# Kernel tuning notes

Hardware: AMD Instinct MI355X
Metric: run time of the kernel (lower is better)

The kernel has to match this reference:

```python
import jax, jax.numpy as jnp
import numpy as np

N_NODES = 100000
N_EDGES = 1600000
IN_DIM = 128
HID_DIM = 32
OUT_DIM = 64
N_REL = 8
N_CLASSES = 2


def setup_inputs() -> dict:
    key = jax.random.key(0)
    ks = jax.random.split(key, 12)
    x = jax.random.normal(ks[0], (N_NODES, IN_DIM), dtype=jnp.float32)
    edge_index = jax.random.randint(ks[1], (2, N_EDGES), 0, N_NODES, dtype=jnp.int64)
    edge_type = jax.random.randint(ks[2], (N_EDGES,), 0, N_REL, dtype=jnp.int64)
    # FastRGCNConv params: per-relation weight W [R, in, out], root weight, bias
    def glorot(k, shape):
        fan_in, fan_out = shape[-2], shape[-1]
        s = jnp.sqrt(6.0 / (fan_in + fan_out))
        return jax.random.uniform(k, shape, jnp.float32, -s, s)
    W1 = glorot(ks[3], (N_REL, IN_DIM, HID_DIM))
    root1 = glorot(ks[4], (IN_DIM, HID_DIM))
    b1 = jnp.zeros((HID_DIM,), jnp.float32)
    W2 = glorot(ks[5], (N_REL, HID_DIM, OUT_DIM))
    root2 = glorot(ks[6], (HID_DIM, OUT_DIM))
    b2 = jnp.zeros((OUT_DIM,), jnp.float32)
    lin_w = glorot(ks[7], (OUT_DIM, N_CLASSES))
    lin_b = jnp.zeros((N_CLASSES,), jnp.float32)
    return {"x": x, "edge_index": edge_index, "edge_type": edge_type,
            "W1": W1, "root1": root1, "b1": b1,
            "W2": W2, "root2": root2, "b2": b2,
            "lin_w": lin_w, "lin_b": lin_b}


def _fast_rgcn_conv(x, W, root, b, src, dst, etype, n_nodes):
    """FastRGCNConv: per-relation transform, gather by (src, relation),
    mean-aggregate by destination, plus root transform and bias."""
    # Transform all nodes by all relation weights: [N, R, H]
    xW = jnp.einsum('nf,rfh->nrh', x, W)
    # Per-edge message: relation-specific transformed source feature [E, H]
    msg = xW[src, etype]
    agg = jax.ops.segment_sum(msg, dst, num_segments=n_nodes)
    deg = jax.ops.segment_sum(jnp.ones((src.shape[0],), x.dtype), dst,
                              num_segments=n_nodes)
    agg = agg / jnp.maximum(deg, 1.0)[:, None]  # mean aggregation
    return agg + x @ root + b


def reference(x, edge_index, edge_type, W1, root1, b1, W2, root2, b2, lin_w, lin_b):
    src, dst = edge_index[0], edge_index[1]
    n = x.shape[0]
    h = jax.nn.relu(_fast_rgcn_conv(x, W1, root1, b1, src, dst, edge_type, n))
    h = _fast_rgcn_conv(h, W2, root2, b2, src, dst, edge_type, n)
    return h @ lin_w + lin_b
```

## Files before the change

### kernel.cpp

```cpp
#include <hip/hip_runtime.h>

#define NN      100000
#define IN_DIM  128
#define HID     32
#define ODIM    64
#define L1C     288
#define L2K     288
#define NWGS    196
#define NCB     784
#define CCAP    40
#define RECCAP  2304
#define G2ST    296
#define PST     40
#define HST     40

using bf16x8 = __attribute__((ext_vector_type(8))) short;
using f32x4  = __attribute__((ext_vector_type(4))) float;

__device__ __forceinline__ float bf2f(short s) {
    unsigned int u = ((unsigned int)(unsigned short)s) << 16;
    float f; __builtin_memcpy(&f, &u, 4); return f;
}
__device__ __forceinline__ short f2bf(float f) {
    unsigned int u; __builtin_memcpy(&u, &f, 4);
    u += 0x7fffu + ((u >> 16) & 1u);
    return (short)(u >> 16);
}
__device__ __forceinline__ float ldf(const void* p, int i, int f32) {
    return f32 ? ((const float*)p)[i] : bf2f(((const short*)p)[i]);
}
__device__ __forceinline__ int ldi(const int* p, long long i, int i64) {
    return i64 ? p[2 * i] : p[(int)i];
}

__global__ __launch_bounds__(1024) void detect(const short* __restrict__ x,
                                               const short* __restrict__ W1,
                                               const short* __restrict__ r1,
                                               const short* __restrict__ W2,
                                               const short* __restrict__ r2,
                                               const short* __restrict__ lw,
                                               const int* __restrict__ ei,
                                               const int* __restrict__ et,
                                               int* __restrict__ flags) {
    __shared__ int cnt[8];
    if (threadIdx.x < 8) cnt[threadIdx.x] = 0;
    __syncthreads();
    const short* ptrs[6] = {x, W1, r1, W2, r2, lw};
    const int    nsmp[6] = {1024, 1024, 1024, 1024, 1024, 64};
    int t = threadIdx.x;
#pragma unroll
    for (int j = 0; j < 6; ++j) {
        if (t < nsmp[j]) {
            unsigned int s = (unsigned short)ptrs[j][2 * t];
            unsigned int e = (s >> 7) & 0xFF;
            if (e >= 140u || (e >= 1u && e <= 100u)) atomicAdd(&cnt[j], 1);
        }
    }
    if (t < 128) {
        if (ei[2 * t + 1] != 0) atomicAdd(&cnt[6], 1);
        if (et[2 * t + 1] != 0) atomicAdd(&cnt[7], 1);
    }
    __syncthreads();
    if (t == 0) {
        const int ns[6] = {1024, 1024, 1024, 1024, 1024, 64};
        for (int j = 0; j < 6; ++j) flags[j] = (cnt[j] * 4 > ns[j]) ? 1 : 0;
        flags[6] = (cnt[6] == 0) ? 1 : 0;
        flags[7] = (cnt[7] == 0) ? 1 : 0;
    }
}

__global__ __launch_bounds__(256) void prep_all(const void* __restrict__ W1,
                                                const void* __restrict__ root1,
                                                const void* __restrict__ W2,
                                                const void* __restrict__ root2,
                                                const short* __restrict__ b1,
                                                const short* __restrict__ b2,
                                                const void* __restrict__ lin_w,
                                                const short* __restrict__ lin_b,
                                                short* __restrict__ w1t,
                                                short* __restrict__ w2ct,
                                                short* __restrict__ smallc,
                                                const int* __restrict__ flags) {
    int gi = blockIdx.x * 256 + threadIdx.x;
    if (gi < L1C * IN_DIM) {
        int c = gi >> 7, f = gi & 127;
        float v;
        if (c < 256) { int r = c >> 5, h = c & 31; v = ldf(W1, (r * IN_DIM + f) * HID + h, flags[1]); }
        else         { v = ldf(root1, f * HID + (c - 256), flags[2]); }
        w1t[c * IN_DIM + f] = f2bf(v);
        return;
    }
    int i2 = gi - L1C * IN_DIM;
    if (i2 < ODIM * L2K) {
        int c = i2 / L2K, k = i2 % L2K;
        float v;
        if (k < 256) { int r = k >> 5, kk = k & 31; v = ldf(W2, (r * HID + kk) * ODIM + c, flags[3]); }
        else         { v = ldf(root2, (k - 256) * ODIM + c, flags[4]); }
        w2ct[c * L2K + k] = f2bf(v);
        return;
    }
    int i3 = i2 - ODIM * L2K;
    if (i3 < 256) {
        if (i3 < 32)        smallc[i3] = b1[i3];
        else if (i3 < 96)   smallc[i3] = b2[i3 - 32];
        else if (i3 < 224)  smallc[i3] = f2bf(ldf(lin_w, i3 - 96, flags[5]));
        else if (i3 < 226)  smallc[i3] = lin_b[i3 - 224];
    }
}

__global__ __launch_bounds__(1024) void scatter_coarse(const int* __restrict__ ei,
                                                       const int* __restrict__ et,
                                                       int* __restrict__ cnt,
                                                       int* __restrict__ seg, int E,
                                                       const int* __restrict__ flags) {
    __shared__ int cur[NCB];
    if (threadIdx.x < NCB) cur[threadIdx.x] = 0;
    __syncthreads();
    int i64 = flags[6], t64 = flags[7];
    int epw = (E + NWGS - 1) / NWGS;
    int lo = blockIdx.x * epw;
    int hi = lo + epw; if (hi > E) hi = E;
    for (int i = lo + threadIdx.x; i < hi; i += 1024) {
        int s = ldi(ei, i, i64);
        int d = ldi(ei, (long long)E + i, i64);
        int r = ldi(et, i, t64);
        int cb = d >> 7;
        int pos = atomicAdd(&cur[cb], 1);
        if (pos < CCAP)
            seg[(cb * NWGS + (int)blockIdx.x) * CCAP + pos] = ((d & 127) << 20) | (s << 3) | r;
    }
    __syncthreads();
    if (threadIdx.x < NCB) {
        int c = cur[threadIdx.x];
        cnt[blockIdx.x * NCB + threadIdx.x] = c < CCAP ? c : CCAP;
    }
}

__global__ __launch_bounds__(64) void cb_sum(const int* __restrict__ cnt,
                                             int* __restrict__ cbTot) {
    int cb = blockIdx.x, lane = threadIdx.x;
    int t = 0;
    for (int g = lane; g < NWGS; g += 64) t += cnt[g * NCB + cb];
#pragma unroll
    for (int o = 32; o > 0; o >>= 1) t += __shfl_down(t, o, 64);
    if (lane == 0) cbTot[cb] = t;
}

__global__ __launch_bounds__(1024) void cb_scan2(const int* __restrict__ cbTot,
                                                 int* __restrict__ cbBase,
                                                 int* __restrict__ off) {
    __shared__ int s[1024];
    int t = threadIdx.x;
    int v = (t < NCB) ? cbTot[t] : 0;
    s[t] = v; __syncthreads();
    for (int o = 1; o < 1024; o <<= 1) {
        int u = (t >= o) ? s[t - o] : 0;
        __syncthreads();
        s[t] += u;
        __syncthreads();
    }
    if (t < NCB) cbBase[t] = s[t] - v;
    if (t == NCB - 1) off[NN] = s[t];
}

__global__ __launch_bounds__(256) void build_cb(const int* __restrict__ cnt,
                                                const int* __restrict__ seg,
                                                const int* __restrict__ cbBase,
                                                int* __restrict__ off,
                                                float* __restrict__ inv_deg,
                                                int* __restrict__ packed) {
    __shared__ int cntl[NWGS], soff[NWGS];
    __shared__ int recs[RECCAP];
    __shared__ int degl[128], basel[128], kcur[128];
    __shared__ int stmp[256];
    int cb = blockIdx.x, tid = threadIdx.x;
    if (tid < NWGS) cntl[tid] = cnt[tid * NCB + cb];
    if (tid < 128) degl[tid] = 0;
    __syncthreads();
    int v = (tid < NWGS) ? cntl[tid] : 0;
    stmp[tid] = v; __syncthreads();
    for (int o = 1; o < 256; o <<= 1) {
        int u = (tid >= o) ? stmp[tid - o] : 0;
        __syncthreads();
        stmp[tid] += u;
        __syncthreads();
    }
    if (tid < NWGS) soff[tid] = stmp[tid] - v;
    int tot = stmp[255]; if (tot > RECCAP) tot = RECCAP;
    __syncthreads();
    int wave = tid >> 6, lane = tid & 63;
    for (int g = wave; g < NWGS; g += 4) {
        int c = cntl[g], b = soff[g];
        const int* sp = seg + (cb * NWGS + g) * CCAP;
        for (int e = lane; e < c; e += 64)
            if (b + e < RECCAP) recs[b + e] = sp[e];
    }
    __syncthreads();
    for (int i = tid; i < tot; i += 256) atomicAdd(&degl[recs[i] >> 20], 1);
    __syncthreads();
    int dv = (tid < 128) ? degl[tid] : 0;
    stmp[tid] = dv; __syncthreads();
    for (int o = 1; o < 128; o <<= 1) {
        int u = (tid >= o) ? stmp[tid - o] : 0;
        __syncthreads();
        stmp[tid] += u;
        __syncthreads();
    }
    int gbase = cbBase[cb];
    if (tid < 128) {
        int excl = stmp[tid] - dv;
        basel[tid] = excl;
        kcur[tid] = 0;
        int node = cb * 128 + tid;
        if (node < NN) {
            off[node] = gbase + excl;
            inv_deg[node] = 1.0f / (float)(dv > 1 ? dv : 1);
        }
    }
    __syncthreads();
    for (int i = tid; i < tot; i += 256) {
        int rec = recs[i];
        int n = rec >> 20;
        int p = atomicAdd(&kcur[n], 1);
        packed[gbase + basel[n] + p] = ((n & 15) << 24) | (rec & 0xFFFFF);
    }
}

__global__ __launch_bounds__(256) void gemm1(const void* __restrict__ x,
                                             const short* __restrict__ w1t,
                                             short* __restrict__ xw,
                                             const int* __restrict__ flags) {
    int wave = threadIdx.x >> 6, lane = threadIdx.x & 63;
    int m = lane & 15, quad = lane >> 4;
    int row0 = (blockIdx.x * 4 + wave) * 64;
    if (row0 >= NN) return;

    bf16x8 a[4][4];
    int fp32 = flags[0];
#pragma unroll
    for (int t = 0; t < 4; ++t) {
        int row = row0 + t * 16 + m;
        int rc = row < NN ? row : NN - 1;
        if (fp32) {
            const float* xr = (const float*)x + rc * IN_DIM + quad * 8;
#pragma unroll
            for (int kt = 0; kt < 4; ++kt) {
                const f32x4* q = (const f32x4*)(xr + kt * 32);
                f32x4 u0 = q[0], u1 = q[1];
                bf16x8 tt;
                tt[0] = f2bf(u0[0]); tt[1] = f2bf(u0[1]); tt[2] = f2bf(u0[2]); tt[3] = f2bf(u0[3]);
                tt[4] = f2bf(u1[0]); tt[5] = f2bf(u1[1]); tt[6] = f2bf(u1[2]); tt[7] = f2bf(u1[3]);
                a[t][kt] = tt;
            }
        } else {
            const short* xr = (const short*)x + rc * IN_DIM + quad * 8;
#pragma unroll
            for (int kt = 0; kt < 4; ++kt) a[t][kt] = *(const bf16x8*)(xr + kt * 32);
        }
    }

    for (int ct = 0; ct < 18; ++ct) {
        const short* wp = w1t + (ct * 16 + m) * IN_DIM + quad * 8;
        bf16x8 b[4];
#pragma unroll
        for (int kt = 0; kt < 4; ++kt) b[kt] = *(const bf16x8*)(wp + kt * 32);
#pragma unroll
        for (int t = 0; t < 4; ++t) {
            f32x4 acc = {0.f, 0.f, 0.f, 0.f};
#pragma unroll
            for (int kt = 0; kt < 4; ++kt)
                acc = __builtin_amdgcn_mfma_f32_16x16x32_bf16(a[t][kt], b[kt], acc, 0, 0, 0);
#pragma unroll
            for (int i = 0; i < 4; ++i) {
                int r = row0 + t * 16 + quad * 4 + i;
                if (r < NN) xw[r * L1C + ct * 16 + m] = f2bf(acc[i]);
            }
        }
    }
}

__global__ __launch_bounds__(256) void agg1(const short* __restrict__ xw,
                                            const int* __restrict__ off,
                                            const int* __restrict__ packed,
                                            const float* __restrict__ inv_deg,
                                            const short* __restrict__ smallc,
                                            short* __restrict__ h) {
    int lane = threadIdx.x & 31;
    int node = blockIdx.x * 8 + (threadIdx.x >> 5);
    if (node >= NN) return;
    int s = off[node], e = off[node + 1];
    float acc = 0.f;
    int i = s;
    for (; i + 7 < e; i += 8) {
        int pk0 = packed[i],     pk1 = packed[i + 1], pk2 = packed[i + 2], pk3 = packed[i + 3];
        int pk4 = packed[i + 4], pk5 = packed[i + 5], pk6 = packed[i + 6], pk7 = packed[i + 7];
        float v0 = bf2f(xw[((pk0 >> 3) & 0x1FFFF) * L1C + (pk0 & 7) * 32 + lane]);
        float v1 = bf2f(xw[((pk1 >> 3) & 0x1FFFF) * L1C + (pk1 & 7) * 32 + lane]);
        float v2 = bf2f(xw[((pk2 >> 3) & 0x1FFFF) * L1C + (pk2 & 7) * 32 + lane]);
        float v3 = bf2f(xw[((pk3 >> 3) & 0x1FFFF) * L1C + (pk3 & 7) * 32 + lane]);
        float v4 = bf2f(xw[((pk4 >> 3) & 0x1FFFF) * L1C + (pk4 & 7) * 32 + lane]);
        float v5 = bf2f(xw[((pk5 >> 3) & 0x1FFFF) * L1C + (pk5 & 7) * 32 + lane]);
        float v6 = bf2f(xw[((pk6 >> 3) & 0x1FFFF) * L1C + (pk6 & 7) * 32 + lane]);
        float v7 = bf2f(xw[((pk7 >> 3) & 0x1FFFF) * L1C + (pk7 & 7) * 32 + lane]);
        acc += ((v0 + v1) + (v2 + v3)) + ((v4 + v5) + (v6 + v7));
    }
    for (; i + 3 < e; i += 4) {
        int pk0 = packed[i], pk1 = packed[i + 1], pk2 = packed[i + 2], pk3 = packed[i + 3];
        float v0 = bf2f(xw[((pk0 >> 3) & 0x1FFFF) * L1C + (pk0 & 7) * 32 + lane]);
        float v1 = bf2f(xw[((pk1 >> 3) & 0x1FFFF) * L1C + (pk1 & 7) * 32 + lane]);
        float v2 = bf2f(xw[((pk2 >> 3) & 0x1FFFF) * L1C + (pk2 & 7) * 32 + lane]);
        float v3 = bf2f(xw[((pk3 >> 3) & 0x1FFFF) * L1C + (pk3 & 7) * 32 + lane]);
        acc += (v0 + v1) + (v2 + v3);
    }
    for (; i < e; ++i) {
        int pk = packed[i];
        acc += bf2f(xw[((pk >> 3) & 0x1FFFF) * L1C + (pk & 7) * 32 + lane]);
    }
    float v = acc * inv_deg[node] + bf2f(xw[node * L1C + 256 + lane]) + bf2f(smallc[lane]);
    h[node * HID + lane] = f2bf(v > 0.f ? v : 0.f);
}

__global__ __launch_bounds__(256) void agg2_fused(const short* __restrict__ h,
                                                  const int* __restrict__ off,
                                                  const int* __restrict__ packed,
                                                  const float* __restrict__ inv_deg,
                                                  const short* __restrict__ w2ct,
                                                  const short* __restrict__ smallc,
                                                  float* __restrict__ out) {
    __shared__ __align__(16) short Pl[128 * PST];
    __shared__ __align__(16) short HgT[32 * HST];
    __shared__ __align__(16) short g2l[16 * G2ST];
    __shared__ float red[4][16][2];
    __shared__ float invl[16];
    int tid = threadIdx.x;
    int row0 = blockIdx.x * 16;
    if (tid < 16) invl[tid] = inv_deg[row0 + tid];
    int st = off[row0], en = off[row0 + 16];

    int wave = tid >> 6, lane = tid & 63;
    int m15 = lane & 15, quad = lane >> 4;
    int e = tid & 31;
    int part = tid >> 5;

    {
        uint4 z = {0, 0, 0, 0};
        uint4* pz = (uint4*)Pl;
#pragma unroll
        for (int j = 0; j < 2; ++j) pz[tid + j * 256] = z;
        if (tid < 128) pz[tid + 512] = z;
    }

    f32x4 acc00 = {0,0,0,0}, acc01 = {0,0,0,0}, acc10 = {0,0,0,0}, acc11 = {0,0,0,0};
    int prevrow = -1;

    for (int c0 = st; c0 < en; c0 += 32) {
        int idx = c0 + e;
        int pk = (idx < en) ? packed[idx] : 0;
        int src = (pk >> 3) & 0x1FFFF;
        uint2 hv = *(const uint2*)(h + src * HID + part * 4);
        __syncthreads();
        if (tid < 32 && prevrow >= 0) Pl[prevrow * PST + e] = 0;
        short hs0 = (short)(hv.x & 0xFFFF), hs1 = (short)(hv.x >> 16);
        short hs2 = (short)(hv.y & 0xFFFF), hs3 = (short)(hv.y >> 16);
        HgT[(part * 4 + 0) * HST + e] = hs0;
        HgT[(part * 4 + 1) * HST + e] = hs1;
        HgT[(part * 4 + 2) * HST + e] = hs2;
        HgT[(part * 4 + 3) * HST + e] = hs3;
        if (tid < 32) {
            if (idx < en) {
                int row = ((pk >> 24) & 15) * 8 + (pk & 7);
                Pl[row * PST + e] = (short)0x3F80;
                prevrow = row;
            } else prevrow = -1;
        }
        __syncthreads();
        bf16x8 a0 = *(const bf16x8*)(&HgT[m15 * HST + quad * 8]);
        bf16x8 a1 = *(const bf16x8*)(&HgT[(m15 + 16) * HST + quad * 8]);
        bf16x8 b0 = *(const bf16x8*)(&Pl[((wave * 2 + 0) * 16 + m15) * PST + quad * 8]);
        bf16x8 b1 = *(const bf16x8*)(&Pl[((wave * 2 + 1) * 16 + m15) * PST + quad * 8]);
        acc00 = __builtin_amdgcn_mfma_f32_16x16x32_bf16(a0, b0, acc00, 0, 0, 0);
        acc10 = __builtin_amdgcn_mfma_f32_16x16x32_bf16(a1, b0, acc10, 0, 0, 0);
        acc01 = __builtin_amdgcn_mfma_f32_16x16x32_bf16(a0, b1, acc01, 0, 0, 0);
        acc11 = __builtin_amdgcn_mfma_f32_16x16x32_bf16(a1, b1, acc11, 0, 0, 0);
    }
    __syncthreads();

    {
        int nr0 = (wave * 2 + 0) * 16 + m15;
        int nr1 = (wave * 2 + 1) * 16 + m15;
        float sc0 = invl[nr0 >> 3], sc1 = invl[nr1 >> 3];
        int d0 = quad * 4;
#pragma unroll
        for (int i = 0; i < 4; ++i) {
            g2l[(nr0 >> 3) * G2ST + (nr0 & 7) * 32 + d0 + i]      = f2bf(acc00[i] * sc0);
            g2l[(nr0 >> 3) * G2ST + (nr0 & 7) * 32 + 16 + d0 + i] = f2bf(acc10[i] * sc0);
            g2l[(nr1 >> 3) * G2ST + (nr1 & 7) * 32 + d0 + i]      = f2bf(acc01[i] * sc1);
            g2l[(nr1 >> 3) * G2ST + (nr1 & 7) * 32 + 16 + d0 + i] = f2bf(acc11[i] * sc1);
        }
    }
    for (int j = tid; j < 16 * 32; j += 256) {
        int node = j >> 5, d = j & 31;
        g2l[node * G2ST + 256 + d] = h[(row0 + node) * HID + d];
    }
    __syncthreads();

    const short* wp = w2ct + (wave * 16 + m15) * L2K + quad * 8;
    bf16x8 a[9], b[9];
#pragma unroll
    for (int kt = 0; kt < 9; ++kt) {
        b[kt] = *(const bf16x8*)(wp + kt * 32);
        a[kt] = *(const bf16x8*)(&g2l[m15 * G2ST + quad * 8 + kt * 32]);
    }
    f32x4 acc = {0.f, 0.f, 0.f, 0.f};
#pragma unroll
    for (int kt = 0; kt < 9; ++kt)
        acc = __builtin_amdgcn_mfma_f32_16x16x32_bf16(a[kt], b[kt], acc, 0, 0, 0);

    int c = wave * 16 + m15;
    float lw0 = bf2f(smallc[96 + c * 2 + 0]);
    float lw1 = bf2f(smallc[96 + c * 2 + 1]);
    float b2c = bf2f(smallc[32 + c]);
    float pr0[4], pr1[4];
#pragma unroll
    for (int i = 0; i < 4; ++i) {
        float v = acc[i] + b2c;
        pr0[i] = v * lw0;
        pr1[i] = v * lw1;
    }
#pragma unroll
    for (int o = 1; o < 16; o <<= 1) {
#pragma unroll
        for (int i = 0; i < 4; ++i) {
            pr0[i] += __shfl_xor(pr0[i], o, 64);
            pr1[i] += __shfl_xor(pr1[i], o, 64);
        }
    }
    if (m15 == 0) {
#pragma unroll
        for (int i = 0; i < 4; ++i) {
            red[wave][quad * 4 + i][0] = pr0[i];
            red[wave][quad * 4 + i][1] = pr1[i];
        }
    }
    __syncthreads();
    if (tid < 32) {
        int row = tid >> 1, j = tid & 1;
        float v = red[0][row][j] + red[1][row][j] + red[2][row][j] + red[3][row][j]
                + bf2f(smallc[224 + j]);
        out[(row0 + row) * 2 + j] = v;
    }
}

extern "C" void kernel_launch(void* const* d_in, const int* in_sizes, int n_in,
                              void* d_out, int out_size, void* d_ws, size_t ws_size,
                              hipStream_t stream) {
    const void* x     = d_in[0];
    const int*  ei    = (const int*)d_in[1];
    const int*  etype = (const int*)d_in[2];
    const void* W1    = d_in[3];
    const void* root1 = d_in[4];
    const void* b1    = d_in[5];
    const void* W2    = d_in[6];
    const void* root2 = d_in[7];
    const void* b2    = d_in[8];
    const void* lin_w = d_in[9];
    const void* lin_b = d_in[10];
    float* out = (float*)d_out;

    const int E = in_sizes[2];

    char* p = (char*)d_ws;
    auto alloc = [&](size_t bytes) { char* r = p; p += (bytes + 255) & ~(size_t)255; return (void*)r; };
    int*   flags   = (int*)  alloc(256);
    int*   off     = (int*)  alloc((size_t)(NN + 1) * 4);
    float* inv_deg = (float*)alloc((size_t)NN * 4);
    int*   packed  = (int*)  alloc((size_t)E * 4);
    int*   cnt     = (int*)  alloc((size_t)NWGS * NCB * 4);
    int*   cbTot   = (int*)  alloc((size_t)NCB * 4);
    int*   cbBase  = (int*)  alloc((size_t)NCB * 4);
    int*   seg     = (int*)  alloc((size_t)NCB * NWGS * CCAP * 4);
    short* w1t     = (short*)alloc((size_t)L1C * IN_DIM * 2);
    short* w2ct    = (short*)alloc((size_t)ODIM * L2K * 2);
    short* smallc  = (short*)alloc(256 * 2);
    short* h       = (short*)alloc((size_t)NN * HID * 2);
    short* xw1     = (short*)alloc((size_t)NN * L1C * 2);

    detect<<<1, 1024, 0, stream>>>((const short*)x, (const short*)W1, (const short*)root1,
                                   (const short*)W2, (const short*)root2, (const short*)lin_w,
                                   ei, etype, flags);
    const int prep_items = L1C * IN_DIM + ODIM * L2K + 256;
    prep_all<<<(prep_items + 255) / 256, 256, 0, stream>>>(W1, root1, W2, root2,
                                                           (const short*)b1, (const short*)b2,
                                                           lin_w, (const short*)lin_b,
                                                           w1t, w2ct, smallc, flags);

    scatter_coarse<<<NWGS, 1024, 0, stream>>>(ei, etype, cnt, seg, E, flags);
    cb_sum<<<NCB, 64, 0, stream>>>(cnt, cbTot);
    cb_scan2<<<1, 1024, 0, stream>>>(cbTot, cbBase, off);
    build_cb<<<NCB, 256, 0, stream>>>(cnt, seg, cbBase, off, inv_deg, packed);

    gemm1<<<((NN + 63) / 64 + 3) / 4, 256, 0, stream>>>(x, w1t, xw1, flags);
    agg1<<<(NN + 7) / 8, 256, 0, stream>>>(xw1, off, packed, inv_deg, smallc, h);
    agg2_fused<<<NN / 16, 256, 0, stream>>>(h, off, packed, inv_deg, w2ct, smallc, out);
}
```

Before: 302.0 us.

## Fold block-base scan into build_cb and process two edge chunks per agg2 iteration

Removes the single-block cb_scan2 launch. Each build_cb block now computes its own global base by reducing cbTot over the preceding blocks and writes off[NN] itself. This trades one serial launch for redundant per-block reductions. agg2_fused now stages two 32-edge chunks per loop iteration using double LDS buffers, which halves the barrier count and lets two gathers be in flight at once, at the cost of more LDS and registers.

```diff
diff --git a/kernel.cpp b/kernel.cpp
--- a/kernel.cpp
+++ b/kernel.cpp
@@ -146,26 +146,9 @@
     if (lane == 0) cbTot[cb] = t;
 }
 
-__global__ __launch_bounds__(1024) void cb_scan2(const int* __restrict__ cbTot,
-                                                 int* __restrict__ cbBase,
-                                                 int* __restrict__ off) {
-    __shared__ int s[1024];
-    int t = threadIdx.x;
-    int v = (t < NCB) ? cbTot[t] : 0;
-    s[t] = v; __syncthreads();
-    for (int o = 1; o < 1024; o <<= 1) {
-        int u = (t >= o) ? s[t - o] : 0;
-        __syncthreads();
-        s[t] += u;
-        __syncthreads();
-    }
-    if (t < NCB) cbBase[t] = s[t] - v;
-    if (t == NCB - 1) off[NN] = s[t];
-}
-
 __global__ __launch_bounds__(256) void build_cb(const int* __restrict__ cnt,
                                                 const int* __restrict__ seg,
-                                                const int* __restrict__ cbBase,
+                                                const int* __restrict__ cbTot,
                                                 int* __restrict__ off,
                                                 float* __restrict__ inv_deg,
                                                 int* __restrict__ packed) {
@@ -173,7 +156,19 @@
     __shared__ int recs[RECCAP];
     __shared__ int degl[128], basel[128], kcur[128];
     __shared__ int stmp[256];
+    __shared__ int gbase_s;
     int cb = blockIdx.x, tid = threadIdx.x;
+    {
+        int part = 0;
+        for (int j = tid; j < cb; j += 256) part += cbTot[j];
+        stmp[tid] = part; __syncthreads();
+        for (int o = 128; o > 0; o >>= 1) {
+            if (tid < o) stmp[tid] += stmp[tid + o];
+            __syncthreads();
+        }
+        if (tid == 0) gbase_s = stmp[0];
+        __syncthreads();
+    }
     if (tid < NWGS) cntl[tid] = cnt[tid * NCB + cb];
     if (tid < 128) degl[tid] = 0;
     __syncthreads();
@@ -206,15 +201,15 @@
         stmp[tid] += u;
         __syncthreads();
     }
-    int gbase = cbBase[cb];
+    int gbase = gbase_s;
     if (tid < 128) {
         int excl = stmp[tid] - dv;
         basel[tid] = excl;
         kcur[tid] = 0;
         int node = cb * 128 + tid;
-        if (node < NN) {
+        if (node <= NN) {
             off[node] = gbase + excl;
-            inv_deg[node] = 1.0f / (float)(dv > 1 ? dv : 1);
+            if (node < NN) inv_deg[node] = 1.0f / (float)(dv > 1 ? dv : 1);
         }
     }
     __syncthreads();
@@ -327,8 +322,8 @@
                                                   const short* __restrict__ w2ct,
                                                   const short* __restrict__ smallc,
                                                   float* __restrict__ out) {
-    __shared__ __align__(16) short Pl[128 * PST];
-    __shared__ __align__(16) short HgT[32 * HST];
+    __shared__ __align__(16) short Pl[2][128 * PST];
+    __shared__ __align__(16) short HgT[2][32 * HST];
     __shared__ __align__(16) short g2l[16 * G2ST];
     __shared__ float red[4][16][2];
     __shared__ float invl[16];
@@ -344,44 +339,64 @@
 
     {
         uint4 z = {0, 0, 0, 0};
-        uint4* pz = (uint4*)Pl;
-#pragma unroll
-        for (int j = 0; j < 2; ++j) pz[tid + j * 256] = z;
-        if (tid < 128) pz[tid + 512] = z;
+        uint4* pz = (uint4*)&Pl[0][0];
+#pragma unroll
+        for (int j = 0; j < 5; ++j) pz[tid + j * 256] = z;
     }
 
     f32x4 acc00 = {0,0,0,0}, acc01 = {0,0,0,0}, acc10 = {0,0,0,0}, acc11 = {0,0,0,0};
-    int prevrow = -1;
-
-    for (int c0 = st; c0 < en; c0 += 32) {
-        int idx = c0 + e;
-        int pk = (idx < en) ? packed[idx] : 0;
-        int src = (pk >> 3) & 0x1FFFF;
-        uint2 hv = *(const uint2*)(h + src * HID + part * 4);
-        __syncthreads();
-        if (tid < 32 && prevrow >= 0) Pl[prevrow * PST + e] = 0;
-        short hs0 = (short)(hv.x & 0xFFFF), hs1 = (short)(hv.x >> 16);
-        short hs2 = (short)(hv.y & 0xFFFF), hs3 = (short)(hv.y >> 16);
-        HgT[(part * 4 + 0) * HST + e] = hs0;
-        HgT[(part * 4 + 1) * HST + e] = hs1;
-        HgT[(part * 4 + 2) * HST + e] = hs2;
-        HgT[(part * 4 + 3) * HST + e] = hs3;
+    int prevrow0 = -1, prevrow1 = -1;
+
+    for (int c0 = st; c0 < en; c0 += 64) {
+        int idx0 = c0 + e, idx1 = c0 + 32 + e;
+        int pk0 = (idx0 < en) ? packed[idx0] : 0;
+        int pk1 = (idx1 < en) ? packed[idx1] : 0;
+        int src0 = (pk0 >> 3) & 0x1FFFF;
+        int src1 = (pk1 >> 3) & 0x1FFFF;
+        uint2 hv0 = *(const uint2*)(h + src0 * HID + part * 4);
+        uint2 hv1 = *(const uint2*)(h + src1 * HID + part * 4);
+        __syncthreads();
         if (tid < 32) {
-            if (idx < en) {
-                int row = ((pk >> 24) & 15) * 8 + (pk & 7);
-                Pl[row * PST + e] = (short)0x3F80;
-                prevrow = row;
-            } else prevrow = -1;
-        }
-        __syncthreads();
-        bf16x8 a0 = *(const bf16x8*)(&HgT[m15 * HST + quad * 8]);
-        bf16x8 a1 = *(const bf16x8*)(&HgT[(m15 + 16) * HST + quad * 8]);
-        bf16x8 b0 = *(const bf16x8*)(&Pl[((wave * 2 + 0) * 16 + m15) * PST + quad * 8]);
-        bf16x8 b1 = *(const bf16x8*)(&Pl[((wave * 2 + 1) * 16 + m15) * PST + quad * 8]);
-        acc00 = __builtin_amdgcn_mfma_f32_16x16x32_bf16(a0, b0, acc00, 0, 0, 0);
-        acc10 = __builtin_amdgcn_mfma_f32_16x16x32_bf16(a1, b0, acc10, 0, 0, 0);
-        acc01 = __builtin_amdgcn_mfma_f32_16x16x32_bf16(a0, b1, acc01, 0, 0, 0);
-        acc11 = __builtin_amdgcn_mfma_f32_16x16x32_bf16(a1, b1, acc11, 0, 0, 0);
+            if (prevrow0 >= 0) Pl[0][prevrow0 * PST + e] = 0;
+            if (prevrow1 >= 0) Pl[1][prevrow1 * PST + e] = 0;
+        }
+        HgT[0][(part * 4 + 0) * HST + e] = (short)(hv0.x & 0xFFFF);
+        HgT[0][(part * 4 + 1) * HST + e] = (short)(hv0.x >> 16);
+        HgT[0][(part * 4 + 2) * HST + e] = (short)(hv0.y & 0xFFFF);
+        HgT[0][(part * 4 + 3) * HST + e] = (short)(hv0.y >> 16);
+        HgT[1][(part * 4 + 0) * HST + e] = (short)(hv1.x & 0xFFFF);
+        HgT[1][(part * 4 + 1) * HST + e] = (short)(hv1.x >> 16);
+        HgT[1][(part * 4 + 2) * HST + e] = (short)(hv1.y & 0xFFFF);
+        HgT[1][(part * 4 + 3) * HST + e] = (short)(hv1.y >> 16);
+        if (tid < 32) {
+            if (idx0 < en) {
+                int row = ((pk0 >> 24) & 15) * 8 + (pk0 & 7);
+                Pl[0][row * PST + e] = (short)0x3F80;
+                prevrow0 = row;
+            } else prevrow0 = -1;
+            if (idx1 < en) {
+                int row = ((pk1 >> 24) & 15) * 8 + (pk1 & 7);
+                Pl[1][row * PST + e] = (short)0x3F80;
+                prevrow1 = row;
+            } else prevrow1 = -1;
+        }
+        __syncthreads();
+        bf16x8 a0c0 = *(const bf16x8*)(&HgT[0][m15 * HST + quad * 8]);
+        bf16x8 a1c0 = *(const bf16x8*)(&HgT[0][(m15 + 16) * HST + quad * 8]);
+        bf16x8 b0c0 = *(const bf16x8*)(&Pl[0][((wave * 2 + 0) * 16 + m15) * PST + quad * 8]);
+        bf16x8 b1c0 = *(const bf16x8*)(&Pl[0][((wave * 2 + 1) * 16 + m15) * PST + quad * 8]);
+        acc00 = __builtin_amdgcn_mfma_f32_16x16x32_bf16(a0c0, b0c0, acc00, 0, 0, 0);
+        acc10 = __builtin_amdgcn_mfma_f32_16x16x32_bf16(a1c0, b0c0, acc10, 0, 0, 0);
+        acc01 = __builtin_amdgcn_mfma_f32_16x16x32_bf16(a0c0, b1c0, acc01, 0, 0, 0);
+        acc11 = __builtin_amdgcn_mfma_f32_16x16x32_bf16(a1c0, b1c0, acc11, 0, 0, 0);
+        bf16x8 a0c1 = *(const bf16x8*)(&HgT[1][m15 * HST + quad * 8]);
+        bf16x8 a1c1 = *(const bf16x8*)(&HgT[1][(m15 + 16) * HST + quad * 8]);
+        bf16x8 b0c1 = *(const bf16x8*)(&Pl[1][((wave * 2 + 0) * 16 + m15) * PST + quad * 8]);
+        bf16x8 b1c1 = *(const bf16x8*)(&Pl[1][((wave * 2 + 1) * 16 + m15) * PST + quad * 8]);
+        acc00 = __builtin_amdgcn_mfma_f32_16x16x32_bf16(a0c1, b0c1, acc00, 0, 0, 0);
+        acc10 = __builtin_amdgcn_mfma_f32_16x16x32_bf16(a1c1, b0c1, acc10, 0, 0, 0);
+        acc01 = __builtin_amdgcn_mfma_f32_16x16x32_bf16(a0c1, b1c1, acc01, 0, 0, 0);
+        acc11 = __builtin_amdgcn_mfma_f32_16x16x32_bf16(a1c1, b1c1, acc11, 0, 0, 0);
     }
     __syncthreads();
 
@@ -477,7 +492,6 @@
     int*   packed  = (int*)  alloc((size_t)E * 4);
     int*   cnt     = (int*)  alloc((size_t)NWGS * NCB * 4);
     int*   cbTot   = (int*)  alloc((size_t)NCB * 4);
-    int*   cbBase  = (int*)  alloc((size_t)NCB * 4);
     int*   seg     = (int*)  alloc((size_t)NCB * NWGS * CCAP * 4);
     short* w1t     = (short*)alloc((size_t)L1C * IN_DIM * 2);
     short* w2ct    = (short*)alloc((size_t)ODIM * L2K * 2);
@@ -496,8 +510,7 @@
 
     scatter_coarse<<<NWGS, 1024, 0, stream>>>(ei, etype, cnt, seg, E, flags);
     cb_sum<<<NCB, 64, 0, stream>>>(cnt, cbTot);
-    cb_scan2<<<1, 1024, 0, stream>>>(cbTot, cbBase, off);
-    build_cb<<<NCB, 256, 0, stream>>>(cnt, seg, cbBase, off, inv_deg, packed);
+    build_cb<<<NCB, 256, 0, stream>>>(cnt, seg, cbTot, off, inv_deg, packed);
 
     gemm1<<<((NN + 63) / 64 + 3) / 4, 256, 0, stream>>>(x, w1t, xw1, flags);
     agg1<<<(NN + 7) / 8, 256, 0, stream>>>(xw1, off, packed, inv_deg, smallc, h);
```

Result: no change. 305.8 us (+1.2%).
